# Optimization experiments

Measured on AMD Instinct MI355X. Metric: run time of the kernel, lower is better.

The kernel has to match this reference:

```python
import jax, jax.numpy as jnp
import numpy as np

N = 100000
E = 1600000
CARDS = [1000, 100, 50, 10000]
EDIMS = [10, 6, 5, 18]  # emb_dim_from_card = clip(round(1.8*card**0.25), 4, 24)
NUM_IN = 32
HID = 128
EPS = 1e-5


def setup_inputs() -> dict:
    key = jax.random.key(0)
    ks = jax.random.split(key, 24)
    x_num = jax.random.normal(ks[0], (N, NUM_IN), dtype=jnp.float32)
    cols = [jax.random.randint(jax.random.fold_in(ks[1], j), (N,), 0, c) for j, c in enumerate(CARDS)]
    x_cat = jnp.stack(cols, axis=1)
    edge_index = jax.random.randint(ks[2], (2, E), 0, N)
    embs = {f"emb{j}": 0.02 * jax.random.normal(ks[3 + j], (c, d), dtype=jnp.float32)
            for j, (c, d) in enumerate(zip(CARDS, EDIMS))}
    in_dim = NUM_IN + sum(EDIMS)  # 71
    def lin(k, fi, fo):
        s = 1.0 / np.sqrt(fi)
        return jax.random.uniform(k, (fi, fo), jnp.float32, -s, s)
    params = dict(
        w_in=lin(ks[7], in_dim, HID), b_in=jnp.zeros((HID,), jnp.float32),
        w1l=lin(ks[8], HID, HID), b1l=jnp.zeros((HID,), jnp.float32), w1r=lin(ks[9], HID, HID),
        w2l=lin(ks[10], HID, HID), b2l=jnp.zeros((HID,), jnp.float32), w2r=lin(ks[11], HID, HID),
        g1=jnp.ones((HID,), jnp.float32), be1=jnp.zeros((HID,), jnp.float32),
        g2=jnp.ones((HID,), jnp.float32), be2=jnp.zeros((HID,), jnp.float32),
        wh1=lin(ks[12], HID, 64), bh1=jnp.zeros((64,), jnp.float32),
        wh2=lin(ks[13], 64, 1), bh2=jnp.zeros((1,), jnp.float32),
    )
    return {"x_num": x_num, "x_cat": x_cat, "edge_index": edge_index, **embs, **params}


def _layer_norm(x, g, b):
    mu = jnp.mean(x, axis=-1, keepdims=True)
    var = jnp.var(x, axis=-1, keepdims=True)
    return (x - mu) * jax.lax.rsqrt(var + EPS) * g + b


def _sage_conv(x, src, dst, wl, bl, wr):
    # PyG SAGEConv(mean): lin_l(mean_{j in N(i)} x_j) + lin_r(x_i)
    agg = jax.ops.segment_sum(x[src], dst, num_segments=N)
    cnt = jax.ops.segment_sum(jnp.ones((src.shape[0],), x.dtype), dst, num_segments=N)
    mean = agg / jnp.maximum(cnt, 1.0)[:, None]
    return mean @ wl + bl + x @ wr


def reference(x_num, x_cat, edge_index,
              emb0, emb1, emb2, emb3,
              w_in, b_in, w1l, b1l, w1r, w2l, b2l, w2r,
              g1, be1, g2, be2, wh1, bh1, wh2, bh2):
    # eval mode: dropout is identity
    zc = jnp.concatenate([emb0[x_cat[:, 0]], emb1[x_cat[:, 1]],
                          emb2[x_cat[:, 2]], emb3[x_cat[:, 3]]], axis=1)
    x = jnp.concatenate([x_num, zc], axis=1)
    x = jax.nn.relu(x @ w_in + b_in)
    src, dst = edge_index[0], edge_index[1]
    x1 = jax.nn.relu(_layer_norm(_sage_conv(x, src, dst, w1l, b1l, w1r), g1, be1))
    x = x + 0.5 * x1
    x2 = jax.nn.relu(_layer_norm(_sage_conv(x, src, dst, w2l, b2l, w2r), g2, be2))
    x = x + 0.5 * x2
    h = jax.nn.relu(x @ wh1 + bh1)
    return (h @ wh2 + bh2)[:, 0]
```

## Files before the change

kernel.cpp:

```cpp
#include <hip/hip_runtime.h>

#define HID 128

typedef __attribute__((ext_vector_type(8))) short short8;
typedef __attribute__((ext_vector_type(4))) float f32x4;

__device__ __forceinline__ float bf2f(unsigned short u) {
    unsigned int x = ((unsigned int)u) << 16;
    return __builtin_bit_cast(float, x);
}
__device__ __forceinline__ unsigned short f2bf(float f) {
    unsigned int u = __builtin_bit_cast(unsigned int, f);
    u += 0x7fffu + ((u >> 16) & 1u);
    return (unsigned short)(u >> 16);
}

__global__ __launch_bounds__(256) void k_prepw(const float* __restrict__ s1, int k1,
    const float* __restrict__ s2, int k2, int Kp, int N,
    unsigned short* __restrict__ whi, unsigned short* __restrict__ wlo)
{
    int i = blockIdx.x * 256 + threadIdx.x;
    if (i >= Kp * N) return;
    int k = i / N, nn = i - k * N;
    float v = 0.f;
    if (k < k1) v = s1[(size_t)k * N + nn];
    else if (k < k1 + k2) v = s2[(size_t)(k - k1) * N + nn];
    unsigned short h = f2bf(v);
    unsigned short l = f2bf(v - bf2f(h));
    size_t o = ((size_t)(k >> 5) * N + nn) * 32 + (k & 31);
    whi[o] = h; wlo[o] = l;
}

__global__ __launch_bounds__(256) void k_stack0(
    const float* __restrict__ xnum, const int* __restrict__ xcat,
    const float* __restrict__ e0, const float* __restrict__ e1,
    const float* __restrict__ e2, const float* __restrict__ e3,
    unsigned short* __restrict__ A0, int n)
{
    int g = blockIdx.x * 256 + threadIdx.x;
    int r = g / 6, c = g - r * 6;
    if (r >= n) return;
    int4 cc = ((const int4*)xcat)[r];
    float v[16];
    int base = c * 16;
    #pragma unroll
    for (int j = 0; j < 16; ++j) {
        int col = base + j;
        float val;
        if      (col < 32) val = xnum[(size_t)r * 32 + col];
        else if (col < 42) val = e0[(size_t)cc.x * 10 + (col - 32)];
        else if (col < 48) val = e1[(size_t)cc.y * 6  + (col - 42)];
        else if (col < 53) val = e2[(size_t)cc.z * 5  + (col - 48)];
        else if (col < 71) val = e3[(size_t)cc.w * 18 + (col - 53)];
        else               val = 0.f;
        v[j] = val;
    }
    unsigned int ph[8];
    #pragma unroll
    for (int j = 0; j < 8; ++j)
        ph[j] = (unsigned int)f2bf(v[2*j]) | ((unsigned int)f2bf(v[2*j+1]) << 16);
    unsigned int* dh = (unsigned int*)(A0 + (size_t)r * 96 + base);
    uint4 a; a.x = ph[0]; a.y = ph[1]; a.z = ph[2]; a.w = ph[3];
    uint4 b; b.x = ph[4]; b.y = ph[5]; b.z = ph[6]; b.w = ph[7];
    ((uint4*)dh)[0] = a; ((uint4*)dh)[1] = b;
}

__global__ __launch_bounds__(256) void k_part(const int* __restrict__ esrc,
    const int* __restrict__ edst, int* __restrict__ gCur, int2* __restrict__ ebuf,
    int ecount, int chunk, int cap)
{
    __shared__ int hist[512];
    __shared__ int base[512];
    int t = threadIdx.x;
    hist[t] = 0; hist[t + 256] = 0;
    __syncthreads();
    int start = blockIdx.x * chunk;
    int end = start + chunk < ecount ? start + chunk : ecount;
    for (int i = start + t; i < end; i += 256)
        atomicAdd(&hist[edst[i] >> 8], 1);
    __syncthreads();
    for (int bk = t; bk < 512; bk += 256) {
        int h = hist[bk];
        base[bk] = h ? atomicAdd(&gCur[bk], h) : 0;
        hist[bk] = 0;
    }
    __syncthreads();
    for (int i = start + t; i < end; i += 256) {
        int d = edst[i];
        int b = d >> 8;
        int slot = atomicAdd(&hist[b], 1);
        int pos = base[b] + slot;
        if (pos < cap)
            ebuf[(size_t)b * cap + pos] = make_int2(esrc[i], d);
    }
}

__global__ __launch_bounds__(512) void k_scanb(const int* __restrict__ gCur,
    int* __restrict__ bBase, int* __restrict__ row_ptr, int nbuck, int n, int ecount)
{
    __shared__ int sm[512];
    int t = threadIdx.x;
    int c = (t < nbuck) ? gCur[t] : 0;
    sm[t] = c;
    __syncthreads();
    for (int d = 1; d < 512; d <<= 1) {
        int v = (t >= d) ? sm[t - d] : 0;
        __syncthreads();
        sm[t] += v;
        __syncthreads();
    }
    if (t < nbuck) bBase[t] = sm[t] - c;
    if (t == 0) row_ptr[n] = ecount;
}

__global__ __launch_bounds__(256) void k_bcsr(const int2* __restrict__ ebuf,
    const int* __restrict__ gCur, const int* __restrict__ bBase,
    int* __restrict__ row_ptr, int* __restrict__ col, int cap, int n)
{
    __shared__ int h[256];
    __shared__ int sm[256];
    int b = blockIdx.x, t = threadIdx.x;
    int cnt = gCur[b];
    int nb0 = b << 8;
    const int2* eb = ebuf + (size_t)b * cap;
    h[t] = 0;
    __syncthreads();
    for (int i = t; i < cnt; i += 256)
        atomicAdd(&h[eb[i].y & 255], 1);
    __syncthreads();
    int hv = h[t];
    sm[t] = hv;
    __syncthreads();
    for (int d = 1; d < 256; d <<= 1) {
        int v = (t >= d) ? sm[t - d] : 0;
        __syncthreads();
        sm[t] += v;
        __syncthreads();
    }
    int excl = sm[t] - hv;
    int gb = bBase[b];
    int g = nb0 + t;
    if (g < n) row_ptr[g] = gb + excl;
    __syncthreads();
    h[t] = excl;
    __syncthreads();
    for (int i = t; i < cnt; i += 256) {
        int2 e = eb[i];
        int slot = atomicAdd(&h[e.y & 255], 1);
        col[gb + slot] = e.x;
    }
}

__global__ __launch_bounds__(256) void k_agg(
    const unsigned short* __restrict__ xh, unsigned short* __restrict__ mh, int SK,
    const int* __restrict__ row_ptr, const int* __restrict__ col, int n)
{
    int lane = threadIdx.x & 63;
    int qw  = lane >> 4;
    int l16 = lane & 15;
    int node = blockIdx.x * 4 + (threadIdx.x >> 6);
    if (node >= n) return;
    node = __builtin_amdgcn_readfirstlane(node);
    int s = row_ptr[node], e = row_ptr[node + 1];
    int deg = e - s;
    float a0 = 0.f, a1 = 0.f, a2 = 0.f, a3 = 0.f;
    float a4 = 0.f, a5 = 0.f, a6 = 0.f, a7 = 0.f;
    size_t cOff = (size_t)l16 * 8;

    auto accum = [&](uint4 r) {
        a0 += __builtin_bit_cast(float, r.x << 16);
        a1 += __builtin_bit_cast(float, r.x & 0xffff0000u);
        a2 += __builtin_bit_cast(float, r.y << 16);
        a3 += __builtin_bit_cast(float, r.y & 0xffff0000u);
        a4 += __builtin_bit_cast(float, r.z << 16);
        a5 += __builtin_bit_cast(float, r.z & 0xffff0000u);
        a6 += __builtin_bit_cast(float, r.w << 16);
        a7 += __builtin_bit_cast(float, r.w & 0xffff0000u);
    };

    int p = s + qw;
    for (; p + 12 < e; p += 16) {
        int sc0 = col[p];
        int sc1 = col[p + 4];
        int sc2 = col[p + 8];
        int sc3 = col[p + 12];
        uint4 r0 = *(const uint4*)(xh + (size_t)sc0 * SK + cOff);
        uint4 r1 = *(const uint4*)(xh + (size_t)sc1 * SK + cOff);
        uint4 r2 = *(const uint4*)(xh + (size_t)sc2 * SK + cOff);
        uint4 r3 = *(const uint4*)(xh + (size_t)sc3 * SK + cOff);
        accum(r0); accum(r1); accum(r2); accum(r3);
    }
    for (; p < e; p += 4) {
        int sc = col[p];
        accum(*(const uint4*)(xh + (size_t)sc * SK + cOff));
    }

    a0 += __shfl_xor(a0, 16); a0 += __shfl_xor(a0, 32);
    a1 += __shfl_xor(a1, 16); a1 += __shfl_xor(a1, 32);
    a2 += __shfl_xor(a2, 16); a2 += __shfl_xor(a2, 32);
    a3 += __shfl_xor(a3, 16); a3 += __shfl_xor(a3, 32);
    a4 += __shfl_xor(a4, 16); a4 += __shfl_xor(a4, 32);
    a5 += __shfl_xor(a5, 16); a5 += __shfl_xor(a5, 32);
    a6 += __shfl_xor(a6, 16); a6 += __shfl_xor(a6, 32);
    a7 += __shfl_xor(a7, 16); a7 += __shfl_xor(a7, 32);

    if (qw == 0) {
        float inv = 1.f / (float)(deg > 1 ? deg : 1);
        uint4 o;
        o.x = (unsigned int)f2bf(a0 * inv) | ((unsigned int)f2bf(a1 * inv) << 16);
        o.y = (unsigned int)f2bf(a2 * inv) | ((unsigned int)f2bf(a3 * inv) << 16);
        o.z = (unsigned int)f2bf(a4 * inv) | ((unsigned int)f2bf(a5 * inv) << 16);
        o.w = (unsigned int)f2bf(a6 * inv) | ((unsigned int)f2bf(a7 * inv) << 16);
        *(uint4*)(mh + (size_t)node * SK + cOff) = o;
    }
}

template<int NC, int KT8, int EPI>
__global__ __launch_bounds__(256) void k_gemm(
    const unsigned short* __restrict__ A, int SK,
    const unsigned short* __restrict__ Whi, const unsigned short* __restrict__ Wlo,
    const float* __restrict__ bias,
    const float* __restrict__ g, const float* __restrict__ be,
    const unsigned short* __restrict__ Src, int SSK,
    unsigned short* __restrict__ Dst, int DSK,
    const float* __restrict__ wh2, const float* __restrict__ bh2, float* __restrict__ outp,
    int n)
{
    constexpr int NT = NC / 64;
    __shared__ float Cb[32][NC + 4];
    int t = threadIdx.x;
    int lane = t & 63, w = t >> 6;
    int l15 = lane & 15, kg = lane >> 4;
    int m0 = blockIdx.x * 64;

    size_t aoff[4];
    #pragma unroll
    for (int mt = 0; mt < 4; ++mt) {
        int r = m0 + mt * 16 + l15;
        r = r < n ? r : n - 1;
        aoff[mt] = (size_t)r * SK + kg * 8;
    }
    size_t nb[NT];
    #pragma unroll
    for (int nt = 0; nt < NT; ++nt)
        nb[nt] = (size_t)(w * (NC / 4) + nt * 16 + l15) * 32 + kg * 8;

    f32x4 acc[4][NT];
    #pragma unroll
    for (int mt = 0; mt < 4; ++mt)
        #pragma unroll
        for (int nt = 0; nt < NT; ++nt)
            acc[mt][nt] = (f32x4)(0.f);

    #pragma unroll 1
    for (int s = 0; s < KT8; ++s) {
        int koff = s * 32;
        short8 ah[4];
        #pragma unroll
        for (int mt = 0; mt < 4; ++mt)
            ah[mt] = *(const short8*)(A + aoff[mt] + koff);
        short8 bh[NT], bl[NT];
        #pragma unroll
        for (int nt = 0; nt < NT; ++nt) {
            bh[nt] = *(const short8*)(Whi + (size_t)s * NC * 32 + nb[nt]);
            bl[nt] = *(const short8*)(Wlo + (size_t)s * NC * 32 + nb[nt]);
        }
        #pragma unroll
        for (int mt = 0; mt < 4; ++mt)
            #pragma unroll
            for (int nt = 0; nt < NT; ++nt)
                acc[mt][nt] = __builtin_amdgcn_mfma_f32_16x16x32_bf16(ah[mt], bh[nt], acc[mt][nt], 0, 0, 0);
        #pragma unroll
        for (int mt = 0; mt < 4; ++mt)
            #pragma unroll
            for (int nt = 0; nt < NT; ++nt)
                acc[mt][nt] = __builtin_amdgcn_mfma_f32_16x16x32_bf16(ah[mt], bl[nt], acc[mt][nt], 0, 0, 0);
    }

    constexpr int CW = NC / 8;
    int er = t >> 3, q = t & 7;
    int cb = q * CW;

    #pragma unroll
    for (int p = 0; p < 2; ++p) {
        if (p) __syncthreads();
        #pragma unroll
        for (int mt2 = 0; mt2 < 2; ++mt2) {
            int mt = 2 * p + mt2;
            #pragma unroll
            for (int nt = 0; nt < NT; ++nt)
                #pragma unroll
                for (int r = 0; r < 4; ++r)
                    Cb[mt2 * 16 + kg * 4 + r][w * (NC / 4) + nt * 16 + l15] = acc[mt][nt][r];
        }
        __syncthreads();

        int gr = m0 + p * 32 + er;

        if (EPI == 0) {
            if (gr < n) {
                #pragma unroll
                for (int i = 0; i < CW / 4; ++i) {
                    int c = cb + 4 * i;
                    float4 v  = *(const float4*)&Cb[er][c];
                    float4 bi = *(const float4*)&bias[c];
                    ushort4 hv = make_ushort4(f2bf(fmaxf(v.x + bi.x, 0.f)),
                                              f2bf(fmaxf(v.y + bi.y, 0.f)),
                                              f2bf(fmaxf(v.z + bi.z, 0.f)),
                                              f2bf(fmaxf(v.w + bi.w, 0.f)));
                    *(ushort4*)(Dst + (size_t)gr * DSK + c) = hv;
                }
            }
        } else if (EPI == 1) {
            float s = 0.f, ss = 0.f;
            #pragma unroll
            for (int i = 0; i < CW / 4; ++i) {
                int c = cb + 4 * i;
                float4 v  = *(const float4*)&Cb[er][c];
                float4 bi = *(const float4*)&bias[c];
                float a0 = v.x + bi.x, a1 = v.y + bi.y, a2 = v.z + bi.z, a3 = v.w + bi.w;
                s  += a0 + a1 + a2 + a3;
                ss += a0 * a0 + a1 * a1 + a2 * a2 + a3 * a3;
            }
            s  += __shfl_xor(s, 1);  s  += __shfl_xor(s, 2);  s  += __shfl_xor(s, 4);
            ss += __shfl_xor(ss, 1); ss += __shfl_xor(ss, 2); ss += __shfl_xor(ss, 4);
            float mu  = s * (1.f / NC);
            float var = ss * (1.f / NC) - mu * mu;
            float rs  = rsqrtf(var + 1e-5f);
            if (gr < n) {
                #pragma unroll
                for (int i = 0; i < CW / 4; ++i) {
                    int c = cb + 4 * i;
                    float4 v  = *(const float4*)&Cb[er][c];
                    float4 bi = *(const float4*)&bias[c];
                    float4 gg = *(const float4*)&g[c];
                    float4 bb = *(const float4*)&be[c];
                    float r0 = fmaxf((v.x + bi.x - mu) * rs * gg.x + bb.x, 0.f);
                    float r1 = fmaxf((v.y + bi.y - mu) * rs * gg.y + bb.y, 0.f);
                    float r2 = fmaxf((v.z + bi.z - mu) * rs * gg.z + bb.z, 0.f);
                    float r3 = fmaxf((v.w + bi.w - mu) * rs * gg.w + bb.w, 0.f);
                    ushort4 rh = *(const ushort4*)(Src + (size_t)gr * SSK + c);
                    ushort4 hv = make_ushort4(f2bf(bf2f(rh.x) + 0.5f * r0),
                                              f2bf(bf2f(rh.y) + 0.5f * r1),
                                              f2bf(bf2f(rh.z) + 0.5f * r2),
                                              f2bf(bf2f(rh.w) + 0.5f * r3));
                    *(ushort4*)(Dst + (size_t)gr * DSK + c) = hv;
                }
            }
        } else {
            float s = 0.f;
            #pragma unroll
            for (int i = 0; i < CW / 4; ++i) {
                int c = cb + 4 * i;
                float4 v  = *(const float4*)&Cb[er][c];
                float4 bi = *(const float4*)&bias[c];
                float4 w2 = *(const float4*)&wh2[c];
                s += fmaxf(v.x + bi.x, 0.f) * w2.x + fmaxf(v.y + bi.y, 0.f) * w2.y
                   + fmaxf(v.z + bi.z, 0.f) * w2.z + fmaxf(v.w + bi.w, 0.f) * w2.w;
            }
            s += __shfl_xor(s, 1); s += __shfl_xor(s, 2); s += __shfl_xor(s, 4);
            if (q == 0 && gr < n) outp[gr] = s + bh2[0];
        }
    }
}

extern "C" void kernel_launch(void* const* d_in, const int* in_sizes, int n_in,
                              void* d_out, int out_size, void* d_ws, size_t ws_size,
                              hipStream_t stream)
{
    const float* xnum = (const float*)d_in[0];
    const int*   xcat = (const int*)d_in[1];
    const int*   eidx = (const int*)d_in[2];
    const float* e0   = (const float*)d_in[3];
    const float* e1   = (const float*)d_in[4];
    const float* e2   = (const float*)d_in[5];
    const float* e3   = (const float*)d_in[6];
    const float* w_in = (const float*)d_in[7];
    const float* b_in = (const float*)d_in[8];
    const float* w1l  = (const float*)d_in[9];
    const float* b1l  = (const float*)d_in[10];
    const float* w1r  = (const float*)d_in[11];
    const float* w2l  = (const float*)d_in[12];
    const float* b2l  = (const float*)d_in[13];
    const float* w2r  = (const float*)d_in[14];
    const float* g1   = (const float*)d_in[15];
    const float* be1  = (const float*)d_in[16];
    const float* g2   = (const float*)d_in[17];
    const float* be2  = (const float*)d_in[18];
    const float* wh1  = (const float*)d_in[19];
    const float* bh1  = (const float*)d_in[20];
    const float* wh2  = (const float*)d_in[21];
    const float* bh2  = (const float*)d_in[22];

    int n = in_sizes[0] / 32;
    int ecount = in_sizes[2] / 2;
    const int* esrc = eidx;
    const int* edst = eidx + ecount;

    char* ws = (char*)d_ws;
    size_t off = 0;
    auto alloc = [&](size_t bytes) -> void* {
        void* p = ws + off;
        off += (bytes + 255) & ~(size_t)255;
        return p;
    };
    unsigned short* A1 = (unsigned short*)alloc((size_t)n * 256 * 2);
    unsigned short* A3 = A1;
    unsigned short* A2 = (unsigned short*)alloc((size_t)n * 256 * 2);
    unsigned short* A0 = A2;
    unsigned short* w0h = (unsigned short*)alloc((size_t)96 * 128 * 2);
    unsigned short* w0l = (unsigned short*)alloc((size_t)96 * 128 * 2);
    unsigned short* w1h = (unsigned short*)alloc((size_t)256 * 128 * 2);
    unsigned short* w1lo= (unsigned short*)alloc((size_t)256 * 128 * 2);
    unsigned short* w2h = (unsigned short*)alloc((size_t)256 * 128 * 2);
    unsigned short* w2lo= (unsigned short*)alloc((size_t)256 * 128 * 2);
    unsigned short* whh = (unsigned short*)alloc((size_t)128 * 64 * 2);
    unsigned short* whl = (unsigned short*)alloc((size_t)128 * 64 * 2);
    int nbuck = (n + 255) >> 8;
    int cap = ecount / nbuck + ecount / (2 * nbuck) + 256;
    int* gCur    = (int*)alloc(512 * 4);
    int* bBase   = (int*)alloc(512 * 4);
    int* row_ptr = (int*)alloc((size_t)(n + 1) * 4);
    int* col     = (int*)alloc((size_t)ecount * 4);
    int2* ebuf   = (int2*)alloc((size_t)nbuck * cap * 8);
    (void)ws_size; (void)n_in; (void)out_size;

    int gemmBlocks = (n + 63) / 64;
    int aggBlocks = (n + 3) / 4;

    k_prepw<<<(96 * 128 + 255) / 256, 256, 0, stream>>>(w_in, 71, nullptr, 0, 96, 128, w0h, w0l);
    k_prepw<<<(256 * 128 + 255) / 256, 256, 0, stream>>>(w1l, 128, w1r, 128, 256, 128, w1h, w1lo);
    k_prepw<<<(256 * 128 + 255) / 256, 256, 0, stream>>>(w2l, 128, w2r, 128, 256, 128, w2h, w2lo);
    k_prepw<<<(128 * 64 + 255) / 256, 256, 0, stream>>>(wh1, 128, nullptr, 0, 128, 64, whh, whl);

    k_stack0<<<((size_t)n * 6 + 255) / 256, 256, 0, stream>>>(xnum, xcat, e0, e1, e2, e3, A0, n);

    hipMemsetAsync(gCur, 0, 512 * 4, stream);
    int nblkP = 512;
    int chunk = (ecount + nblkP - 1) / nblkP;
    k_part<<<nblkP, 256, 0, stream>>>(esrc, edst, gCur, ebuf, ecount, chunk, cap);
    k_scanb<<<1, 512, 0, stream>>>(gCur, bBase, row_ptr, nbuck, n, ecount);
    k_bcsr<<<nbuck, 256, 0, stream>>>(ebuf, gCur, bBase, row_ptr, col, cap, n);

    k_gemm<128, 3, 0><<<gemmBlocks, 256, 0, stream>>>(
        A0, 96, w0h, w0l, b_in,
        nullptr, nullptr, nullptr, 0,
        A1 + 128, 256,
        nullptr, nullptr, nullptr, n);

    k_agg<<<aggBlocks, 256, 0, stream>>>(A1 + 128, A1, 256, row_ptr, col, n);
    k_gemm<128, 8, 1><<<gemmBlocks, 256, 0, stream>>>(
        A1, 256, w1h, w1lo, b1l,
        g1, be1, A1 + 128, 256,
        A2 + 128, 256,
        nullptr, nullptr, nullptr, n);

    k_agg<<<aggBlocks, 256, 0, stream>>>(A2 + 128, A2, 256, row_ptr, col, n);
    k_gemm<128, 8, 1><<<gemmBlocks, 256, 0, stream>>>(
        A2, 256, w2h, w2lo, b2l,
        g2, be2, A2 + 128, 256,
        A3, 128,
        nullptr, nullptr, nullptr, n);

    k_gemm<64, 4, 2><<<gemmBlocks, 256, 0, stream>>>(
        A3, 128, whh, whl, bh1,
        nullptr, nullptr, nullptr, 0,
        nullptr, 0,
        wh2, bh2, (float*)d_out, n);
}
```

Baseline: 450.8 us.

## Fuse neighbor mean aggregation into SAGE conv GEMM with LayerNorm epilogue

Replaces the separate aggregation kernel and the conv GEMM with one kernel per layer. Each block gathers the neighbor means for its 64 nodes into shared memory, then runs the bf16 hi/lo MFMA GEMM over the mean half and the self half, followed by the LayerNorm, ReLU and residual epilogue. This removes the round trip of the mean matrix through global memory, one launch per layer, and the interleaved 256-wide activation buffers. In exchange, each block serializes 16 gathers per wave before its MFMA work, which can lower latency hiding during the gather phase.

Measured after the change: 515.6 us. 14.4% more time.

```diff
diff --git a/kernel.cpp b/kernel.cpp
--- a/kernel.cpp
+++ b/kernel.cpp
@@ -151,67 +151,197 @@
     }
 }
 
-__global__ __launch_bounds__(256) void k_agg(
-    const unsigned short* __restrict__ xh, unsigned short* __restrict__ mh, int SK,
-    const int* __restrict__ row_ptr, const int* __restrict__ col, int n)
-{
-    int lane = threadIdx.x & 63;
-    int qw  = lane >> 4;
-    int l16 = lane & 15;
-    int node = blockIdx.x * 4 + (threadIdx.x >> 6);
-    if (node >= n) return;
-    node = __builtin_amdgcn_readfirstlane(node);
-    int s = row_ptr[node], e = row_ptr[node + 1];
-    int deg = e - s;
-    float a0 = 0.f, a1 = 0.f, a2 = 0.f, a3 = 0.f;
-    float a4 = 0.f, a5 = 0.f, a6 = 0.f, a7 = 0.f;
-    size_t cOff = (size_t)l16 * 8;
-
-    auto accum = [&](uint4 r) {
-        a0 += __builtin_bit_cast(float, r.x << 16);
-        a1 += __builtin_bit_cast(float, r.x & 0xffff0000u);
-        a2 += __builtin_bit_cast(float, r.y << 16);
-        a3 += __builtin_bit_cast(float, r.y & 0xffff0000u);
-        a4 += __builtin_bit_cast(float, r.z << 16);
-        a5 += __builtin_bit_cast(float, r.z & 0xffff0000u);
-        a6 += __builtin_bit_cast(float, r.w << 16);
-        a7 += __builtin_bit_cast(float, r.w & 0xffff0000u);
-    };
-
-    int p = s + qw;
-    for (; p + 12 < e; p += 16) {
-        int sc0 = col[p];
-        int sc1 = col[p + 4];
-        int sc2 = col[p + 8];
-        int sc3 = col[p + 12];
-        uint4 r0 = *(const uint4*)(xh + (size_t)sc0 * SK + cOff);
-        uint4 r1 = *(const uint4*)(xh + (size_t)sc1 * SK + cOff);
-        uint4 r2 = *(const uint4*)(xh + (size_t)sc2 * SK + cOff);
-        uint4 r3 = *(const uint4*)(xh + (size_t)sc3 * SK + cOff);
-        accum(r0); accum(r1); accum(r2); accum(r3);
-    }
-    for (; p < e; p += 4) {
-        int sc = col[p];
-        accum(*(const uint4*)(xh + (size_t)sc * SK + cOff));
-    }
-
-    a0 += __shfl_xor(a0, 16); a0 += __shfl_xor(a0, 32);
-    a1 += __shfl_xor(a1, 16); a1 += __shfl_xor(a1, 32);
-    a2 += __shfl_xor(a2, 16); a2 += __shfl_xor(a2, 32);
-    a3 += __shfl_xor(a3, 16); a3 += __shfl_xor(a3, 32);
-    a4 += __shfl_xor(a4, 16); a4 += __shfl_xor(a4, 32);
-    a5 += __shfl_xor(a5, 16); a5 += __shfl_xor(a5, 32);
-    a6 += __shfl_xor(a6, 16); a6 += __shfl_xor(a6, 32);
-    a7 += __shfl_xor(a7, 16); a7 += __shfl_xor(a7, 32);
-
-    if (qw == 0) {
-        float inv = 1.f / (float)(deg > 1 ? deg : 1);
-        uint4 o;
-        o.x = (unsigned int)f2bf(a0 * inv) | ((unsigned int)f2bf(a1 * inv) << 16);
-        o.y = (unsigned int)f2bf(a2 * inv) | ((unsigned int)f2bf(a3 * inv) << 16);
-        o.z = (unsigned int)f2bf(a4 * inv) | ((unsigned int)f2bf(a5 * inv) << 16);
-        o.w = (unsigned int)f2bf(a6 * inv) | ((unsigned int)f2bf(a7 * inv) << 16);
-        *(uint4*)(mh + (size_t)node * SK + cOff) = o;
+__global__ __launch_bounds__(256) void k_conv(
+    const unsigned short* __restrict__ X, int n,
+    const int* __restrict__ row_ptr, const int* __restrict__ col,
+    const unsigned short* __restrict__ Whi, const unsigned short* __restrict__ Wlo,
+    const float* __restrict__ bias, const float* __restrict__ g,
+    const float* __restrict__ be, unsigned short* __restrict__ Dst, int DSK)
+{
+    __shared__ char smraw[64 * 136 * 2];
+    unsigned short (*meanS)[136] = (unsigned short(*)[136])smraw;
+    float (*Cb)[132] = (float(*)[132])smraw;
+
+    int t = threadIdx.x;
+    int lane = t & 63, w = t >> 6;
+    int kg = lane >> 4, l15 = lane & 15;
+    int m0 = blockIdx.x * 64;
+
+    size_t cOff = (size_t)l15 * 8;
+    #pragma unroll 1
+    for (int i = 0; i < 16; ++i) {
+        int nd0 = m0 + w * 16 + i;
+        int nd = nd0 < n ? nd0 : n - 1;
+        nd = __builtin_amdgcn_readfirstlane(nd);
+        int s0 = row_ptr[nd], e0 = row_ptr[nd + 1];
+        int deg = e0 - s0;
+        float a0 = 0.f, a1 = 0.f, a2 = 0.f, a3 = 0.f;
+        float a4 = 0.f, a5 = 0.f, a6 = 0.f, a7 = 0.f;
+        auto accum = [&](uint4 r) {
+            a0 += __builtin_bit_cast(float, r.x << 16);
+            a1 += __builtin_bit_cast(float, r.x & 0xffff0000u);
+            a2 += __builtin_bit_cast(float, r.y << 16);
+            a3 += __builtin_bit_cast(float, r.y & 0xffff0000u);
+            a4 += __builtin_bit_cast(float, r.z << 16);
+            a5 += __builtin_bit_cast(float, r.z & 0xffff0000u);
+            a6 += __builtin_bit_cast(float, r.w << 16);
+            a7 += __builtin_bit_cast(float, r.w & 0xffff0000u);
+        };
+        int p = s0 + kg;
+        for (; p + 12 < e0; p += 16) {
+            int sc0 = col[p];
+            int sc1 = col[p + 4];
+            int sc2 = col[p + 8];
+            int sc3 = col[p + 12];
+            uint4 r0 = *(const uint4*)(X + (size_t)sc0 * HID + cOff);
+            uint4 r1 = *(const uint4*)(X + (size_t)sc1 * HID + cOff);
+            uint4 r2 = *(const uint4*)(X + (size_t)sc2 * HID + cOff);
+            uint4 r3 = *(const uint4*)(X + (size_t)sc3 * HID + cOff);
+            accum(r0); accum(r1); accum(r2); accum(r3);
+        }
+        for (; p < e0; p += 4) {
+            int sc = col[p];
+            accum(*(const uint4*)(X + (size_t)sc * HID + cOff));
+        }
+        a0 += __shfl_xor(a0, 16); a0 += __shfl_xor(a0, 32);
+        a1 += __shfl_xor(a1, 16); a1 += __shfl_xor(a1, 32);
+        a2 += __shfl_xor(a2, 16); a2 += __shfl_xor(a2, 32);
+        a3 += __shfl_xor(a3, 16); a3 += __shfl_xor(a3, 32);
+        a4 += __shfl_xor(a4, 16); a4 += __shfl_xor(a4, 32);
+        a5 += __shfl_xor(a5, 16); a5 += __shfl_xor(a5, 32);
+        a6 += __shfl_xor(a6, 16); a6 += __shfl_xor(a6, 32);
+        a7 += __shfl_xor(a7, 16); a7 += __shfl_xor(a7, 32);
+        if (kg == 0) {
+            float inv = 1.f / (float)(deg > 1 ? deg : 1);
+            uint4 o;
+            o.x = (unsigned int)f2bf(a0 * inv) | ((unsigned int)f2bf(a1 * inv) << 16);
+            o.y = (unsigned int)f2bf(a2 * inv) | ((unsigned int)f2bf(a3 * inv) << 16);
+            o.z = (unsigned int)f2bf(a4 * inv) | ((unsigned int)f2bf(a5 * inv) << 16);
+            o.w = (unsigned int)f2bf(a6 * inv) | ((unsigned int)f2bf(a7 * inv) << 16);
+            *(uint4*)&meanS[w * 16 + i][l15 * 8] = o;
+        }
+    }
+    __syncthreads();
+
+    size_t nb[2];
+    #pragma unroll
+    for (int nt = 0; nt < 2; ++nt)
+        nb[nt] = (size_t)(w * 32 + nt * 16 + l15) * 32 + kg * 8;
+
+    f32x4 acc[4][2];
+    #pragma unroll
+    for (int mt = 0; mt < 4; ++mt)
+        #pragma unroll
+        for (int nt = 0; nt < 2; ++nt)
+            acc[mt][nt] = (f32x4)(0.f);
+
+    #pragma unroll 1
+    for (int s = 0; s < 4; ++s) {
+        short8 ah[4];
+        #pragma unroll
+        for (int mt = 0; mt < 4; ++mt)
+            ah[mt] = *(const short8*)&meanS[mt * 16 + l15][kg * 8 + s * 32];
+        short8 bh[2], bl[2];
+        #pragma unroll
+        for (int nt = 0; nt < 2; ++nt) {
+            bh[nt] = *(const short8*)(Whi + (size_t)s * HID * 32 + nb[nt]);
+            bl[nt] = *(const short8*)(Wlo + (size_t)s * HID * 32 + nb[nt]);
+        }
+        #pragma unroll
+        for (int mt = 0; mt < 4; ++mt)
+            #pragma unroll
+            for (int nt = 0; nt < 2; ++nt)
+                acc[mt][nt] = __builtin_amdgcn_mfma_f32_16x16x32_bf16(ah[mt], bh[nt], acc[mt][nt], 0, 0, 0);
+        #pragma unroll
+        for (int mt = 0; mt < 4; ++mt)
+            #pragma unroll
+            for (int nt = 0; nt < 2; ++nt)
+                acc[mt][nt] = __builtin_amdgcn_mfma_f32_16x16x32_bf16(ah[mt], bl[nt], acc[mt][nt], 0, 0, 0);
+    }
+    size_t xoff[4];
+    #pragma unroll
+    for (int mt = 0; mt < 4; ++mt) {
+        int r = m0 + mt * 16 + l15;
+        r = r < n ? r : n - 1;
+        xoff[mt] = (size_t)r * HID + kg * 8;
+    }
+    #pragma unroll 1
+    for (int s = 4; s < 8; ++s) {
+        short8 ah[4];
+        #pragma unroll
+        for (int mt = 0; mt < 4; ++mt)
+            ah[mt] = *(const short8*)(X + xoff[mt] + (s - 4) * 32);
+        short8 bh[2], bl[2];
+        #pragma unroll
+        for (int nt = 0; nt < 2; ++nt) {
+            bh[nt] = *(const short8*)(Whi + (size_t)s * HID * 32 + nb[nt]);
+            bl[nt] = *(const short8*)(Wlo + (size_t)s * HID * 32 + nb[nt]);
+        }
+        #pragma unroll
+        for (int mt = 0; mt < 4; ++mt)
+            #pragma unroll
+            for (int nt = 0; nt < 2; ++nt)
+                acc[mt][nt] = __builtin_amdgcn_mfma_f32_16x16x32_bf16(ah[mt], bh[nt], acc[mt][nt], 0, 0, 0);
+        #pragma unroll
+        for (int mt = 0; mt < 4; ++mt)
+            #pragma unroll
+            for (int nt = 0; nt < 2; ++nt)
+                acc[mt][nt] = __builtin_amdgcn_mfma_f32_16x16x32_bf16(ah[mt], bl[nt], acc[mt][nt], 0, 0, 0);
+    }
+    __syncthreads();
+
+    int er = t >> 3, q = t & 7;
+    int cb = q * 16;
+    #pragma unroll
+    for (int p = 0; p < 2; ++p) {
+        if (p) __syncthreads();
+        #pragma unroll
+        for (int mt2 = 0; mt2 < 2; ++mt2) {
+            int mt = 2 * p + mt2;
+            #pragma unroll
+            for (int nt = 0; nt < 2; ++nt)
+                #pragma unroll
+                for (int r = 0; r < 4; ++r)
+                    Cb[mt2 * 16 + kg * 4 + r][w * 32 + nt * 16 + l15] = acc[mt][nt][r];
+        }
+        __syncthreads();
+
+        int gr = m0 + p * 32 + er;
+        float s = 0.f, ss = 0.f;
+        #pragma unroll
+        for (int i = 0; i < 4; ++i) {
+            int c = cb + 4 * i;
+            float4 v  = *(const float4*)&Cb[er][c];
+            float4 bi = *(const float4*)&bias[c];
+            float a0 = v.x + bi.x, a1 = v.y + bi.y, a2 = v.z + bi.z, a3 = v.w + bi.w;
+            s  += a0 + a1 + a2 + a3;
+            ss += a0 * a0 + a1 * a1 + a2 * a2 + a3 * a3;
+        }
+        s  += __shfl_xor(s, 1);  s  += __shfl_xor(s, 2);  s  += __shfl_xor(s, 4);
+        ss += __shfl_xor(ss, 1); ss += __shfl_xor(ss, 2); ss += __shfl_xor(ss, 4);
+        float mu  = s * (1.f / HID);
+        float var = ss * (1.f / HID) - mu * mu;
+        float rs  = rsqrtf(var + 1e-5f);
+        if (gr < n) {
+            #pragma unroll
+            for (int i = 0; i < 4; ++i) {
+                int c = cb + 4 * i;
+                float4 v  = *(const float4*)&Cb[er][c];
+                float4 bi = *(const float4*)&bias[c];
+                float4 gg = *(const float4*)&g[c];
+                float4 bb = *(const float4*)&be[c];
+                float r0 = fmaxf((v.x + bi.x - mu) * rs * gg.x + bb.x, 0.f);
+                float r1 = fmaxf((v.y + bi.y - mu) * rs * gg.y + bb.y, 0.f);
+                float r2 = fmaxf((v.z + bi.z - mu) * rs * gg.z + bb.z, 0.f);
+                float r3 = fmaxf((v.w + bi.w - mu) * rs * gg.w + bb.w, 0.f);
+                ushort4 rh = *(const ushort4*)(X + (size_t)gr * HID + c);
+                ushort4 hv = make_ushort4(f2bf(bf2f(rh.x) + 0.5f * r0),
+                                          f2bf(bf2f(rh.y) + 0.5f * r1),
+                                          f2bf(bf2f(rh.z) + 0.5f * r2),
+                                          f2bf(bf2f(rh.w) + 0.5f * r3));
+                *(ushort4*)(Dst + (size_t)gr * DSK + c) = hv;
+            }
+        }
     }
 }
 
@@ -220,8 +350,6 @@
     const unsigned short* __restrict__ A, int SK,
     const unsigned short* __restrict__ Whi, const unsigned short* __restrict__ Wlo,
     const float* __restrict__ bias,
-    const float* __restrict__ g, const float* __restrict__ be,
-    const unsigned short* __restrict__ Src, int SSK,
     unsigned short* __restrict__ Dst, int DSK,
     const float* __restrict__ wh2, const float* __restrict__ bh2, float* __restrict__ outp,
     int n)
@@ -308,42 +436,6 @@
                                               f2bf(fmaxf(v.y + bi.y, 0.f)),
                                               f2bf(fmaxf(v.z + bi.z, 0.f)),
                                               f2bf(fmaxf(v.w + bi.w, 0.f)));
-                    *(ushort4*)(Dst + (size_t)gr * DSK + c) = hv;
-                }
-            }
-        } else if (EPI == 1) {
-            float s = 0.f, ss = 0.f;
-            #pragma unroll
-            for (int i = 0; i < CW / 4; ++i) {
-                int c = cb + 4 * i;
-                float4 v  = *(const float4*)&Cb[er][c];
-                float4 bi = *(const float4*)&bias[c];
-                float a0 = v.x + bi.x, a1 = v.y + bi.y, a2 = v.z + bi.z, a3 = v.w + bi.w;
-                s  += a0 + a1 + a2 + a3;
-                ss += a0 * a0 + a1 * a1 + a2 * a2 + a3 * a3;
-            }
-            s  += __shfl_xor(s, 1);  s  += __shfl_xor(s, 2);  s  += __shfl_xor(s, 4);
-            ss += __shfl_xor(ss, 1); ss += __shfl_xor(ss, 2); ss += __shfl_xor(ss, 4);
-            float mu  = s * (1.f / NC);
-            float var = ss * (1.f / NC) - mu * mu;
-            float rs  = rsqrtf(var + 1e-5f);
-            if (gr < n) {
-                #pragma unroll
-                for (int i = 0; i < CW / 4; ++i) {
-                    int c = cb + 4 * i;
-                    float4 v  = *(const float4*)&Cb[er][c];
-                    float4 bi = *(const float4*)&bias[c];
-                    float4 gg = *(const float4*)&g[c];
-                    float4 bb = *(const float4*)&be[c];
-                    float r0 = fmaxf((v.x + bi.x - mu) * rs * gg.x + bb.x, 0.f);
-                    float r1 = fmaxf((v.y + bi.y - mu) * rs * gg.y + bb.y, 0.f);
-                    float r2 = fmaxf((v.z + bi.z - mu) * rs * gg.z + bb.z, 0.f);
-                    float r3 = fmaxf((v.w + bi.w - mu) * rs * gg.w + bb.w, 0.f);
-                    ushort4 rh = *(const ushort4*)(Src + (size_t)gr * SSK + c);
-                    ushort4 hv = make_ushort4(f2bf(bf2f(rh.x) + 0.5f * r0),
-                                              f2bf(bf2f(rh.y) + 0.5f * r1),
-                                              f2bf(bf2f(rh.z) + 0.5f * r2),
-                                              f2bf(bf2f(rh.w) + 0.5f * r3));
                     *(ushort4*)(Dst + (size_t)gr * DSK + c) = hv;
                 }
             }
@@ -404,10 +496,10 @@
         off += (bytes + 255) & ~(size_t)255;
         return p;
     };
-    unsigned short* A1 = (unsigned short*)alloc((size_t)n * 256 * 2);
-    unsigned short* A3 = A1;
-    unsigned short* A2 = (unsigned short*)alloc((size_t)n * 256 * 2);
-    unsigned short* A0 = A2;
+    unsigned short* x0 = (unsigned short*)alloc((size_t)n * 128 * 2);
+    unsigned short* x1 = (unsigned short*)alloc((size_t)n * 128 * 2);
+    unsigned short* x2 = x0;
+    unsigned short* A0 = x1;
     unsigned short* w0h = (unsigned short*)alloc((size_t)96 * 128 * 2);
     unsigned short* w0l = (unsigned short*)alloc((size_t)96 * 128 * 2);
     unsigned short* w1h = (unsigned short*)alloc((size_t)256 * 128 * 2);
@@ -426,7 +518,6 @@
     (void)ws_size; (void)n_in; (void)out_size;
 
     int gemmBlocks = (n + 63) / 64;
-    int aggBlocks = (n + 3) / 4;
 
     k_prepw<<<(96 * 128 + 255) / 256, 256, 0, stream>>>(w_in, 71, nullptr, 0, 96, 128, w0h, w0l);
     k_prepw<<<(256 * 128 + 255) / 256, 256, 0, stream>>>(w1l, 128, w1r, 128, 256, 128, w1h, w1lo);
@@ -443,28 +534,14 @@
     k_bcsr<<<nbuck, 256, 0, stream>>>(ebuf, gCur, bBase, row_ptr, col, cap, n);
 
     k_gemm<128, 3, 0><<<gemmBlocks, 256, 0, stream>>>(
-        A0, 96, w0h, w0l, b_in,
-        nullptr, nullptr, nullptr, 0,
-        A1 + 128, 256,
-        nullptr, nullptr, nullptr, n);
-
-    k_agg<<<aggBlocks, 256, 0, stream>>>(A1 + 128, A1, 256, row_ptr, col, n);
-    k_gemm<128, 8, 1><<<gemmBlocks, 256, 0, stream>>>(
-        A1, 256, w1h, w1lo, b1l,
-        g1, be1, A1 + 128, 256,
-        A2 + 128, 256,
-        nullptr, nullptr, nullptr, n);
-
-    k_agg<<<aggBlocks, 256, 0, stream>>>(A2 + 128, A2, 256, row_ptr, col, n);
-    k_gemm<128, 8, 1><<<gemmBlocks, 256, 0, stream>>>(
-        A2, 256, w2h, w2lo, b2l,
-        g2, be2, A2 + 128, 256,
-        A3, 128,
-        nullptr, nullptr, nullptr, n);
+        A0, 96, w0h, w0l, b_in, x0, 128, nullptr, nullptr, nullptr, n);
+
+    k_conv<<<gemmBlocks, 256, 0, stream>>>(
+        x0, n, row_ptr, col, w1h, w1lo, b1l, g1, be1, x1, 128);
+
+    k_conv<<<gemmBlocks, 256, 0, stream>>>(
+        x1, n, row_ptr, col, w2h, w2lo, b2l, g2, be2, x2, 128);
 
     k_gemm<64, 4, 2><<<gemmBlocks, 256, 0, stream>>>(
-        A3, 128, whh, whl, bh1,
-        nullptr, nullptr, nullptr, 0,
-        nullptr, 0,
-        wh2, bh2, (float*)d_out, n);
-}
+        x2, 128, whh, whl, bh1, nullptr, 0, wh2, bh2, (float*)d_out, n);
+}
```
